# Optimization experiments

Measured on AMD Instinct MI355X. Metric: run time of the kernel, lower is better.

Reference implementation:

```python
import jax, jax.numpy as jnp
import numpy as np

B, T, C, H = 4, 1024, 512, 4
D = C // H
N_LAYER, LAYER_ID = 12, 1


def setup_inputs() -> dict:
    key = jax.random.key(0)
    ks = jax.random.split(key, 10)
    w = lambda k, shape: 0.02 * jax.random.normal(k, shape, dtype=jnp.float32)

    r01 = LAYER_ID / (N_LAYER - 1)          # ratio_0_to_1
    r1a0 = 1.0 - LAYER_ID / N_LAYER          # ratio_1_to_almost0
    i = np.arange(C, dtype=np.float32)
    time_decay = (-5.0 + 8.0 * (i / (C - 1)) ** (0.7 + 1.3 * r01)).astype(np.float32)
    xv = i / C
    tm_q = (xv ** r1a0).astype(np.float32)[None, None, :]
    tm_k = (xv ** r1a0).astype(np.float32)[None, None, :]
    tm_v = ((xv ** r1a0) + 0.3 * r01).astype(np.float32)[None, None, :]
    tm_g = (xv ** (0.5 * r1a0)).astype(np.float32)[None, None, :]

    return dict(
        x=jax.random.normal(ks[0], (B, T, C), dtype=jnp.float32),
        ln1_g=jnp.ones((C,), jnp.float32), ln1_b=jnp.zeros((C,), jnp.float32),
        ln2_g=jnp.ones((C,), jnp.float32), ln2_b=jnp.zeros((C,), jnp.float32),
        time_decay=jnp.asarray(time_decay),
        tm_q=jnp.asarray(tm_q), tm_k=jnp.asarray(tm_k),
        tm_v=jnp.asarray(tm_v), tm_g=jnp.asarray(tm_g),
        Wq=w(ks[1], (C, C)), Wk=w(ks[2], (C, C)), Wv=w(ks[3], (C, C)),
        Wg=w(ks[4], (C, C)), Wo=w(ks[5], (C, C)),
        rms_scale=jnp.ones((C,), jnp.float32),
        W1=w(ks[6], (4 * C, C)), W2=w(ks[7], (C, 4 * C)),
    )


def layernorm(x, g, b, eps=1e-5):
    m = x.mean(-1, keepdims=True)
    v = ((x - m) ** 2).mean(-1, keepdims=True)
    return g * (x - m) / jnp.sqrt(v + eps) + b


def rmsnorm(x, scale, eps=1e-8):
    # matches: norm = ||x||_2 / sqrt(dim); out = scale * x / (norm + eps)
    norm = jnp.sqrt(jnp.sum(x * x, axis=-1, keepdims=True)) / (x.shape[-1] ** 0.5)
    return scale * (x / (norm + eps))


def lnssm_scan(q, k, v, lam):
    """Decayed linear-attention scan. q,k,v: [B,T,H,D]; lam: [H,D] (decay over k index).
    Returns S: [B,T,H,D] = q_t^T A_t, Zs: [B,T,H] = q_t . z_t."""
    qT, kT, vT = (jnp.moveaxis(a, 1, 0) for a in (q, k, v))  # [T,B,H,D]
    Bq = q.shape[0]
    A0 = jnp.zeros((Bq, q.shape[2], q.shape[3], q.shape[3]), q.dtype)
    z0 = jnp.zeros((Bq, q.shape[2], q.shape[3]), q.dtype)

    def step(carry, inp):
        A, z = carry
        qt, kt, vt = inp
        A = lam[None, :, :, None] * A + kt[..., None] * vt[..., None, :]  # [B,H,Dk,Dv]
        z = lam[None] * z + kt                                            # [B,H,Dk]
        St = jnp.einsum('bhi,bhij->bhj', qt, A)
        Zt = jnp.einsum('bhi,bhi->bh', qt, z)
        return (A, z), (St, Zt)

    _, (S, Zs) = jax.lax.scan(step, (A0, z0), (qT, kT, vT))
    return jnp.moveaxis(S, 0, 1), jnp.moveaxis(Zs, 0, 1)


def reference(x, ln1_g, ln1_b, ln2_g, ln2_b, time_decay, tm_q, tm_k, tm_v, tm_g,
              Wq, Wk, Wv, Wg, Wo, rms_scale, W1, W2):
    Bx, Tx, Cx = x.shape
    Hh, Dd = H, Cx // H

    # --- TimeMix on ln1(x) ---
    h = layernorm(x, ln1_g, ln1_b)
    xx = jnp.concatenate([jnp.zeros_like(h[:, :1]), h[:, :-1]], axis=1)  # time shift
    xq = h * tm_q + xx * (1 - tm_q)
    xk = h * tm_k + xx * (1 - tm_k)
    xv_ = h * tm_v + xx * (1 - tm_v)
    xg = h * tm_g + xx * (1 - tm_g)
    q = xq @ Wq.T
    k = xk @ Wk.T
    v = xv_ @ Wv.T
    g = jax.nn.sigmoid(xg @ Wg.T)
    q = jnp.exp(rmsnorm(q, rms_scale))
    k = jnp.exp(rmsnorm(k, rms_scale))

    lam = jnp.exp(-jnp.exp(time_decay)).reshape(Hh, Dd)
    qh = q.reshape(Bx, Tx, Hh, Dd)
    kh = k.reshape(Bx, Tx, Hh, Dd)
    vh = v.reshape(Bx, Tx, Hh, Dd)
    S, Zs = lnssm_scan(qh, kh, vh, lam)
    att = (S / Zs[..., None]).reshape(Bx, Tx, Cx)
    att = (g * att) @ Wo.T
    x = x + att

    # --- ChannelMix on ln2(x) ---
    h2 = layernorm(x, ln2_g, ln2_b)
    x = x + jax.nn.gelu(h2 @ W1.T, approximate=False) @ W2.T
    return x
```

## Files before the change

kernel.cpp:

```cpp
#include <hip/hip_runtime.h>
#include <math.h>

#define Bb 4
#define Tt 1024
#define Cc 512
#define Hh 4
#define Dd 128
#define Mrows (Bb*Tt)
#define NC 32
#define CL 32
#define AUGB_CB 18432

typedef unsigned short u16;
typedef __attribute__((ext_vector_type(8))) short bf16x8;
typedef __attribute__((ext_vector_type(4))) float f32x4;

__device__ __forceinline__ u16 f2bf(float f) {
  unsigned u = __float_as_uint(f);
  unsigned r = (u + 0x7fffu + ((u >> 16) & 1u)) >> 16;
  return (u16)r;
}
__device__ __forceinline__ float bf2f(u16 v) {
  return __uint_as_float((unsigned)v << 16);
}
__device__ __forceinline__ unsigned pack2(float a, float b) {
  return (unsigned)f2bf(a) | ((unsigned)f2bf(b) << 16);
}
__device__ __forceinline__ float rms_r(const float* __restrict__ ssqp, int zsel, int row) {
  const float* p = ssqp + (size_t)zsel*8*Mrows + row;
  float s2 = 0.f;
  #pragma unroll
  for (int u = 0; u < 8; ++u) s2 += p[(size_t)u*Mrows];
  float norm = sqrtf(s2) * 0.044194173824159216f;
  return 1.f / (norm + 1e-8f);
}

__global__ __launch_bounds__(256) void prep_kernel(const float* __restrict__ x,
    const float* __restrict__ g, const float* __restrict__ bta,
    const float* __restrict__ tmq, const float* __restrict__ tmk,
    const float* __restrict__ tmv, const float* __restrict__ tmg,
    u16* __restrict__ xqb, u16* __restrict__ xkb,
    u16* __restrict__ xvb, u16* __restrict__ xgb,
    const float* __restrict__ Wq, const float* __restrict__ Wk,
    const float* __restrict__ Wv, const float* __restrict__ Wg,
    const float* __restrict__ Wo, const float* __restrict__ W1,
    const float* __restrict__ W2, u16* __restrict__ wout)
{
  int tid = threadIdx.x;
  if (blockIdx.x >= 4096) {
    int blk = blockIdx.x - 4096;
    const float* src; u16* dst; int K, nshift;
    if (blk < 640) {
      int wsel = blk >> 7;
      src = wsel==0?Wq:wsel==1?Wk:wsel==2?Wv:wsel==3?Wg:Wo;
      dst = wout + (size_t)wsel*262144; K = 512; nshift = 9; blk &= 127;
    } else if (blk < 1152) {
      src = W1; dst = wout + (size_t)5*262144; K = 512; nshift = 11; blk -= 640;
    } else {
      src = W2; dst = wout + (size_t)5*262144 + 1048576; K = 2048; nshift = 9; blk -= 1152;
    }
    int i = blk*256 + tid;
    int n = i & ((1 << nshift) - 1), kg = i >> nshift;
    const float* p = src + (size_t)n * K + kg * 8;
    float4 a = *(const float4*)p, b = *(const float4*)(p + 4);
    uint4 o;
    o.x = pack2(a.x, a.y); o.y = pack2(a.z, a.w);
    o.z = pack2(b.x, b.y); o.w = pack2(b.z, b.w);
    *(uint4*)(dst + (size_t)i * 8) = o;
    return;
  }
  int m = blockIdx.x;
  const float* xr = x + (size_t)m * Cc;
  float v0 = xr[tid], v1 = xr[tid + 256];
  bool has = (m & (Tt-1)) != 0;
  float u0 = 0.f, u1 = 0.f;
  if (has) { u0 = xr[tid - Cc]; u1 = xr[(int)tid + 256 - Cc]; }
  float sa = v0 + v1, qa = v0*v0 + v1*v1;
  float sb = u0 + u1, qb = u0*u0 + u1*u1;
  #pragma unroll
  for (int off = 32; off > 0; off >>= 1) {
    sa += __shfl_down(sa, off, 64); qa += __shfl_down(qa, off, 64);
    sb += __shfl_down(sb, off, 64); qb += __shfl_down(qb, off, 64);
  }
  __shared__ float r4[4][4];
  int w = tid >> 6;
  if ((tid & 63) == 0) { r4[w][0]=sa; r4[w][1]=qa; r4[w][2]=sb; r4[w][3]=qb; }
  __syncthreads();
  float Sa = r4[0][0]+r4[1][0]+r4[2][0]+r4[3][0];
  float Qa = r4[0][1]+r4[1][1]+r4[2][1]+r4[3][1];
  float Sb = r4[0][2]+r4[1][2]+r4[2][2]+r4[3][2];
  float Qb = r4[0][3]+r4[1][3]+r4[2][3]+r4[3][3];
  float ma = Sa*(1.f/Cc), va = Qa*(1.f/Cc) - ma*ma, ia = rsqrtf(va + 1e-5f);
  float mb = Sb*(1.f/Cc), vb = Qb*(1.f/Cc) - mb*mb, ib = rsqrtf(vb + 1e-5f);
  #pragma unroll
  for (int half = 0; half < 2; ++half) {
    int c = tid + half*256;
    float v = half ? v1 : v0, u = half ? u1 : u0;
    float hv = g[c]*(v - ma)*ia + bta[c];
    float pv = has ? (g[c]*(u - mb)*ib + bta[c]) : 0.f;
    size_t off = ((size_t)(c >> 3) * Mrows + m) * 8 + (c & 7);
    float tq = tmq[c], tk = tmk[c], tv = tmv[c], tg = tmg[c];
    xqb[off] = f2bf(hv*tq + pv*(1.f-tq));
    xkb[off] = f2bf(hv*tk + pv*(1.f-tk));
    xvb[off] = f2bf(hv*tv + pv*(1.f-tv));
    xgb[off] = f2bf(hv*tg + pv*(1.f-tg));
  }
}

__global__ __launch_bounds__(256) void ln2b_kernel(const float* __restrict__ x,
    const float* __restrict__ p0,
    const float* __restrict__ g, const float* __restrict__ bta,
    float* __restrict__ x1, u16* __restrict__ out)
{
  int row = blockIdx.x, tid = threadIdx.x;
  size_t r0 = (size_t)row * Cc + tid, r1 = r0 + 256;
  float v0 = x[r0] + p0[r0];
  float v1 = x[r1] + p0[r1];
  x1[r0] = v0; x1[r1] = v1;
  float s = v0 + v1, s2 = v0*v0 + v1*v1;
  #pragma unroll
  for (int off = 32; off > 0; off >>= 1) {
    s  += __shfl_down(s,  off, 64);
    s2 += __shfl_down(s2, off, 64);
  }
  __shared__ float rs[4], rq[4];
  int w = tid >> 6;
  if ((tid & 63) == 0) { rs[w] = s; rq[w] = s2; }
  __syncthreads();
  float S  = rs[0]+rs[1]+rs[2]+rs[3];
  float S2 = rq[0]+rq[1]+rq[2]+rq[3];
  float mean = S * (1.0f/Cc);
  float var  = S2 * (1.0f/Cc) - mean*mean;
  float inv = rsqrtf(var + 1e-5f);
  int c0 = tid, c1 = tid + 256;
  float o0 = g[c0] * (v0-mean)*inv + bta[c0];
  float o1 = g[c1] * (v1-mean)*inv + bta[c1];
  out[((size_t)(c0 >> 3) * Mrows + row) * 8 + (c0 & 7)] = f2bf(o0);
  out[((size_t)(c1 >> 3) * Mrows + row) * 8 + (c1 & 7)] = f2bf(o1);
}

template<int MR, int NR, int KR>
__device__ __forceinline__ void gemm_core64(const u16* __restrict__ A,
    const u16* __restrict__ W, const float* __restrict__ res,
    float* __restrict__ outf, u16* __restrict__ outb, int act,
    int m0, int n0, u16* Asm, u16* Bsm, float* __restrict__ ssq)
{
  const int tid = threadIdx.x, w = tid >> 6, l = tid & 63;
  const int wr = w >> 1, wc = w & 1;
  f32x4 acc[2][2];
  #pragma unroll
  for (int i = 0; i < 2; ++i)
    #pragma unroll
    for (int j = 0; j < 2; ++j) acc[i][j] = (f32x4){0.f,0.f,0.f,0.f};
  const int kgl = l >> 4, rl = l & 15;
  const int q = w * 2;

  #define STAGE(KT, BUF) do {                                               \
    _Pragma("unroll")                                                       \
    for (int ii = 0; ii < 2; ++ii) {                                        \
      int qq = q + ii;                                                      \
      int isB = qq >> 2, kg = qq & 3;                                       \
      const u16* src = isB                                                  \
        ? W + ((size_t)((KT)*4 + kg) * NR + n0 + l) * 8                     \
        : A + ((size_t)((KT)*4 + kg) * MR + m0 + l) * 8;                    \
      u16* dst = (isB ? Bsm : Asm) + (BUF)*2048 + kg * 64 * 8;              \
      __builtin_amdgcn_global_load_lds(                                     \
          (const __attribute__((address_space(1))) void*)src,               \
          (__attribute__((address_space(3))) void*)dst, 16, 0, 0);          \
    }                                                                       \
  } while (0)

  constexpr int nk = KR >> 5;
  STAGE(0, 0); STAGE(1, 1);
  int cur = 0;
  for (int kt = 0; kt < nk; ++kt) {
    if (kt == nk - 1) asm volatile("s_waitcnt vmcnt(0)" ::: "memory");
    else              asm volatile("s_waitcnt vmcnt(2)" ::: "memory");
    __builtin_amdgcn_s_barrier();
    bf16x8 af[2], bfr[2];
    #pragma unroll
    for (int f = 0; f < 2; ++f)
      af[f] = *(const bf16x8*)&Asm[cur*2048 + (kgl*64 + wr*32 + f*16 + rl) * 8];
    #pragma unroll
    for (int f = 0; f < 2; ++f)
      bfr[f] = *(const bf16x8*)&Bsm[cur*2048 + (kgl*64 + wc*32 + f*16 + rl) * 8];
    if (kt + 2 < nk) {
      int nb = cur + 2; if (nb >= 3) nb -= 3;
      STAGE(kt + 2, nb);
    }
    __builtin_amdgcn_s_setprio(1);
    #pragma unroll
    for (int i = 0; i < 2; ++i)
      #pragma unroll
      for (int j = 0; j < 2; ++j)
        acc[i][j] = __builtin_amdgcn_mfma_f32_16x16x32_bf16(af[i], bfr[j], acc[i][j], 0, 0, 0);
    __builtin_amdgcn_s_setprio(0);
    if (++cur == 3) cur = 0;
  }
  #undef STAGE

  const int rbase = (l >> 4) * 4, cn = l & 15;
  #pragma unroll
  for (int i = 0; i < 2; ++i) {
    #pragma unroll
    for (int j = 0; j < 2; ++j) {
      #pragma unroll
      for (int r = 0; r < 4; ++r) {
        int m = m0 + wr*32 + i*16 + rbase + r;
        int n = n0 + wc*32 + j*16 + cn;
        float vv = acc[i][j][r];
        if (res) vv += res[(size_t)m * NR + n];
        if (act == 1) vv = 0.5f*vv*(1.f + erff(vv * 0.70710678118f));
        else if (act == 2) vv = 1.f/(1.f + expf(-vv));
        if (outb) outb[((size_t)(n >> 3) * MR + m) * 8 + (n & 7)] = f2bf(vv);
        else outf[(size_t)m * NR + n] = vv;
      }
    }
  }

  if (ssq) {
    __syncthreads();
    float* red2 = (float*)Asm;
    #pragma unroll
    for (int i = 0; i < 2; ++i) {
      #pragma unroll
      for (int r = 0; r < 4; ++r) {
        int row_local = wr*32 + i*16 + rbase + r;
        float sq = 0.f;
        #pragma unroll
        for (int j = 0; j < 2; ++j) { float t = acc[i][j][r]; sq += t*t; }
        red2[row_local*32 + wc*16 + cn] = sq;
      }
    }
    __syncthreads();
    if (tid < 64) {
      float ssum = 0.f;
      #pragma unroll
      for (int u2 = 0; u2 < 32; ++u2) ssum += red2[tid*32 + u2];
      ssq[m0 + tid] = ssum;
    }
  }
}

__global__ __launch_bounds__(256) void gemm_qkvg(const u16* __restrict__ xall,
    const u16* __restrict__ Wall, float* __restrict__ outall, float* __restrict__ ssqp)
{
  __shared__ __align__(16) u16 Asm[3*2048];
  __shared__ __align__(16) u16 Bsm[3*2048];
  int z = blockIdx.z;
  const size_t E = (size_t)Mrows * Cc;
  float* ssq = (z < 2) ? ssqp + ((size_t)z*8 + blockIdx.x)*Mrows : nullptr;
  gemm_core64<Mrows,512,512>(xall + z*E, Wall + (size_t)z*262144, nullptr,
            outall + z*E, nullptr, z == 3 ? 2 : 0,
            blockIdx.y * 64, blockIdx.x * 64, Asm, Bsm, ssq);
}

__global__ __launch_bounds__(256) void gemm_wo(const u16* __restrict__ A,
    const u16* __restrict__ W, float* __restrict__ outf)
{
  __shared__ __align__(16) u16 Asm[3*2048];
  __shared__ __align__(16) u16 Bsm[3*2048];
  gemm_core64<Mrows,512,512>(A, W, nullptr, outf, nullptr, 0,
            blockIdx.y * 64, blockIdx.x * 64, Asm, Bsm, nullptr);
}

__global__ __launch_bounds__(256) void gemm_w1(const u16* __restrict__ A,
    const u16* __restrict__ W, u16* __restrict__ outb)
{
  __shared__ __align__(16) u16 Asm[3*2048];
  __shared__ __align__(16) u16 Bsm[3*2048];
  gemm_core64<Mrows,2048,512>(A, W, nullptr, nullptr, outb, 1,
            blockIdx.y * 64, blockIdx.x * 64, Asm, Bsm, nullptr);
}

__global__ __launch_bounds__(256) void gemm_w2(const u16* __restrict__ A,
    const u16* __restrict__ W, float* __restrict__ pbuf)
{
  __shared__ __align__(16) u16 Asm[3*2048];
  __shared__ __align__(16) u16 Bsm[3*2048];
  int z = blockIdx.z;
  const size_t E = (size_t)Mrows * Cc;
  gemm_core64<Mrows,512,1024>(A + (size_t)z*128*Mrows*8, W + (size_t)z*128*512*8, nullptr,
            pbuf + z*E, nullptr, 0, blockIdx.y * 64, blockIdx.x * 64, Asm, Bsm, nullptr);
}

__global__ __launch_bounds__(256) void reduce2_kernel(const float* __restrict__ x1,
    const float* __restrict__ p, float* __restrict__ out)
{
  const size_t E = (size_t)Mrows * Cc;
  size_t f = ((size_t)blockIdx.x * 256 + threadIdx.x) * 4;
  float4 a = *(const float4*)(x1 + f);
  float4 q0 = *(const float4*)(p + f);
  float4 q1 = *(const float4*)(p + E + f);
  float4 o;
  o.x = a.x + q0.x + q1.x;
  o.y = a.y + q0.y + q1.y;
  o.z = a.z + q0.z + q1.z;
  o.w = a.w + q0.w + q1.w;
  *(float4*)(out + f) = o;
}

__global__ __launch_bounds__(256) void chunk_state_kernel(const float* __restrict__ k,
    const float* __restrict__ v, const float* __restrict__ td,
    const float* __restrict__ rsc, const float* __restrict__ ssqp,
    u16* __restrict__ Augl)
{
  __shared__ float k_lds[CL][Dd];
  __shared__ float v_lds[CL][Dd];
  int blk = blockIdx.x; int c = blk & (NC-1); int bh = blk >> 5;
  int b = bh >> 2, h = bh & 3;
  int tid = threadIdx.x;
  size_t base = ((size_t)b*Tt + (size_t)c*CL)*Cc + h*Dd;
  #pragma unroll
  for (int r = 0; r < 4; ++r) {
    int idx4 = r*256 + tid;
    int s = idx4 >> 5; int i4 = (idx4 & 31) << 2;
    float rk = rms_r(ssqp, 1, b*Tt + c*CL + s);
    float4 kr = *(const float4*)&k[base + (size_t)s*Cc + i4];
    k_lds[s][i4+0] = expf(rsc[h*Dd+i4+0] * kr.x * rk);
    k_lds[s][i4+1] = expf(rsc[h*Dd+i4+1] * kr.y * rk);
    k_lds[s][i4+2] = expf(rsc[h*Dd+i4+2] * kr.z * rk);
    k_lds[s][i4+3] = expf(rsc[h*Dd+i4+3] * kr.w * rk);
    *(float4*)&v_lds[s][i4] = *(const float4*)&v[base + (size_t)s*Cc + i4];
  }
  __syncthreads();
  int iq = tid >> 3; int i0 = iq << 2;
  int jg = tid & 7;  int j0 = jg << 4;
  float lam4[4], powv[4], zacc[4];
  #pragma unroll
  for (int ci=0; ci<4; ++ci) {
    lam4[ci] = expf(-expf(td[h*Dd + i0 + ci]));
    powv[ci] = 1.f; zacc[ci] = 0.f;
  }
  float acc[4][16];
  #pragma unroll
  for (int ci=0; ci<4; ++ci)
    #pragma unroll
    for (int jj=0; jj<16; ++jj) acc[ci][jj] = 0.f;

  for (int s = CL-1; s >= 0; --s) {
    float4 k4 = *(const float4*)&k_lds[s][i0];
    float kw0 = powv[0]*k4.x, kw1 = powv[1]*k4.y, kw2 = powv[2]*k4.z, kw3 = powv[3]*k4.w;
    zacc[0]+=kw0; zacc[1]+=kw1; zacc[2]+=kw2; zacc[3]+=kw3;
    #pragma unroll
    for (int q4 = 0; q4 < 4; ++q4) {
      float4 v4 = *(const float4*)&v_lds[s][j0 + q4*4];
      float vv[4] = {v4.x, v4.y, v4.z, v4.w};
      #pragma unroll
      for (int u=0; u<4; ++u) {
        acc[0][q4*4+u] += kw0*vv[u];
        acc[1][q4*4+u] += kw1*vv[u];
        acc[2][q4*4+u] += kw2*vv[u];
        acc[3][q4*4+u] += kw3*vv[u];
      }
    }
    powv[0]*=lam4[0]; powv[1]*=lam4[1]; powv[2]*=lam4[2]; powv[3]*=lam4[3];
  }
  u16* aug = Augl + ((size_t)c*16 + bh)*AUGB_CB;
  const int ig = i0 >> 3, isub = i0 & 7;
  #pragma unroll
  for (int jj=0; jj<16; ++jj) {
    int j = j0 + jj;
    uint2 pk;
    pk.x = pack2(acc[0][jj], acc[1][jj]);
    pk.y = pack2(acc[2][jj], acc[3][jj]);
    *(uint2*)&aug[(size_t)ig*1152 + (size_t)j*8 + isub] = pk;
  }
  if (jg == 0) {
    uint2 pk;
    pk.x = pack2(zacc[0], zacc[1]);
    pk.y = pack2(zacc[2], zacc[3]);
    *(uint2*)&aug[(size_t)ig*1152 + 128*8 + isub] = pk;
  }
}

__global__ __launch_bounds__(256) void combine_kernel(const u16* __restrict__ Augl,
    const float* __restrict__ td, u16* __restrict__ Augb)
{
  int idx = blockIdx.x*256 + threadIdx.x;
  if (idx >= 129*128) return;
  int bh = blockIdx.y; int h = bh & 3;
  int j = idx >> 7, i = idx & 127;
  size_t aoff = (size_t)(i >> 3) * 1152 + (size_t)j * 8 + (i & 7);
  float lamL = expf(-expf(td[h*Dd + i]) * (float)CL);
  const u16* pl = Augl + (size_t)bh*AUGB_CB + aoff;
  u16* pi = Augb + (size_t)bh*AUGB_CB + aoff;
  float prev = 0.f;
  const size_t cstr = (size_t)16*AUGB_CB;
  for (int c = 0; c < NC; ++c) {
    float val = bf2f(pl[c*cstr]);
    pi[c*cstr] = f2bf(prev);
    prev = lamL*prev + val;
  }
}

__global__ __launch_bounds__(256, 2) void scan_mfma_kernel(
    const float* __restrict__ q, const float* __restrict__ k,
    const float* __restrict__ v, const float* __restrict__ td,
    const float* __restrict__ rsc, const float* __restrict__ ssqp,
    const u16* __restrict__ Augb, const float* __restrict__ gmat,
    u16* __restrict__ out)
{
  __shared__ float k_lds[32*192];
  __shared__ u16  qfrag[32*128];
  __shared__ u16  vfrag[4*1152];
  __shared__ float P32[32*33];
  __shared__ u16  pfrag[32*32];
  __shared__ float lam_lds[128];
  __shared__ float zbuf[32];

  const int tid = threadIdx.x;
  const int blk = blockIdx.x; const int c = blk & 31, bh = blk >> 5;
  const int b = bh >> 2, h = bh & 3;
  const int w = tid >> 6, l = tid & 63;
  const int t = (w << 3) + (l >> 3);
  const int is = l & 7;

  if (tid < 128) lam_lds[tid] = expf(-expf(td[h*Dd + tid]));

  const int grow = b*Tt + c*CL + t;
  const size_t rowbase = ((size_t)grow)*Cc + h*Dd + is*16;
  const float rq = rms_r(ssqp, 0, grow);
  const float rk = rms_r(ssqp, 1, grow);

  float qv[16];
  {
    #pragma unroll
    for (int c4 = 0; c4 < 4; ++c4) {
      float4 q4 = *(const float4*)(q + rowbase + c4*4);
      int e0 = c4*4;
      qv[e0+0] = expf(rsc[h*Dd+is*16+e0+0] * q4.x * rq);
      qv[e0+1] = expf(rsc[h*Dd+is*16+e0+1] * q4.y * rq);
      qv[e0+2] = expf(rsc[h*Dd+is*16+e0+2] * q4.z * rq);
      qv[e0+3] = expf(rsc[h*Dd+is*16+e0+3] * q4.w * rq);
    }
    float lt = (float)(t + 1);
    u16 qt[16];
    #pragma unroll
    for (int e = 0; e < 16; ++e) {
      float el2 = -expf(td[h*Dd + is*16 + e]) * 1.4426950408889634f;
      qt[e] = f2bf(qv[e] * exp2f(el2 * lt));
    }
    #pragma unroll
    for (int hf = 0; hf < 2; ++hf) {
      int k8 = is*2 + hf;
      uint4 pk;
      pk.x = (unsigned)qt[hf*8+0] | ((unsigned)qt[hf*8+1]<<16);
      pk.y = (unsigned)qt[hf*8+2] | ((unsigned)qt[hf*8+3]<<16);
      pk.z = (unsigned)qt[hf*8+4] | ((unsigned)qt[hf*8+5]<<16);
      pk.w = (unsigned)qt[hf*8+6] | ((unsigned)qt[hf*8+7]<<16);
      *(uint4*)&qfrag[t*128 + ((k8 ^ (t&7))<<3)] = pk;
    }
  }
  #pragma unroll
  for (int c4 = 0; c4 < 4; ++c4) {
    float4 k4 = *(const float4*)(k + rowbase + c4*4);
    int e0 = is*16 + c4*4;
    k_lds[t*192 + is*24 + c4*4+0] = expf(rsc[h*Dd+e0+0] * k4.x * rk);
    k_lds[t*192 + is*24 + c4*4+1] = expf(rsc[h*Dd+e0+1] * k4.y * rk);
    k_lds[t*192 + is*24 + c4*4+2] = expf(rsc[h*Dd+e0+2] * k4.z * rk);
    k_lds[t*192 + is*24 + c4*4+3] = expf(rsc[h*Dd+e0+3] * k4.w * rk);
  }
  #pragma unroll
  for (int c4 = 0; c4 < 4; ++c4) {
    float4 v4 = *(const float4*)(v + rowbase + c4*4);
    int j0 = is*16 + c4*4;
    vfrag[(t>>3)*1152 + (j0+0)*8 + (t&7)] = f2bf(v4.x);
    vfrag[(t>>3)*1152 + (j0+1)*8 + (t&7)] = f2bf(v4.y);
    vfrag[(t>>3)*1152 + (j0+2)*8 + (t&7)] = f2bf(v4.z);
    vfrag[(t>>3)*1152 + (j0+3)*8 + (t&7)] = f2bf(v4.w);
  }
  if (tid < 32) vfrag[(tid>>3)*1152 + 128*8 + (tid&7)] = 0x3F80;
  if (tid < 240) {
    #pragma unroll
    for (int u = 0; u < 2; ++u) {
      int e = tid*2 + u;
      int ig = e / 120, rem = e % 120;
      vfrag[ig*1152 + (129 + rem/8)*8 + (rem&7)] = 0;
    }
  }
  __syncthreads();

  {
    float lamr[16], wrun[16];
    #pragma unroll
    for (int e4 = 0; e4 < 4; ++e4) {
      float4 l4 = *(const float4*)&lam_lds[is*16 + e4*4];
      lamr[e4*4+0]=l4.x; lamr[e4*4+1]=l4.y; lamr[e4*4+2]=l4.z; lamr[e4*4+3]=l4.w;
    }
    #pragma unroll
    for (int e = 0; e < 16; ++e) wrun[e] = 1.f;
    const int smax = (w << 3) + 7;
    for (int s = smax; s >= 0; --s) {
      float dot = 0.f;
      #pragma unroll
      for (int c4 = 0; c4 < 4; ++c4) {
        float4 k4 = *(const float4*)&k_lds[s*192 + is*24 + c4*4];
        dot = fmaf(qv[c4*4+0], k4.x*wrun[c4*4+0], dot);
        dot = fmaf(qv[c4*4+1], k4.y*wrun[c4*4+1], dot);
        dot = fmaf(qv[c4*4+2], k4.z*wrun[c4*4+2], dot);
        dot = fmaf(qv[c4*4+3], k4.w*wrun[c4*4+3], dot);
      }
      dot += __shfl_xor(dot, 1);
      dot += __shfl_xor(dot, 2);
      dot += __shfl_xor(dot, 4);
      bool act = (s <= t);
      if (act && is == 0) P32[t*33 + s] = dot;
      if (act) {
        #pragma unroll
        for (int e = 0; e < 16; ++e) wrun[e] *= lamr[e];
      }
    }
  }
  __syncthreads();
  {
    int tt = tid >> 3, s0 = (tid & 7) * 4;
    #pragma unroll
    for (int ss = 0; ss < 4; ++ss) {
      int s = s0 + ss;
      float val = (s <= tt) ? P32[tt*33 + s] : 0.f;
      pfrag[tt*32 + (((s>>3) ^ (tt&3))<<3) + (s&7)] = f2bf(val);
    }
  }
  __syncthreads();

  const int tau = w >> 1;
  const int jt0 = (w & 1) ? 5 : 0;
  const int njt = (w & 1) ? 4 : 5;
  const int rl = l & 15, kg = l >> 4;
  const int trow = tau*16 + rl;
  const u16* augb_base = Augb + ((size_t)c*16 + bh)*AUGB_CB;

  bf16x8 aq[4];
  #pragma unroll
  for (int kk = 0; kk < 4; ++kk)
    aq[kk] = *(const bf16x8*)&qfrag[trow*128 + ((((kk<<2)+kg) ^ (trow&7))<<3)];
  bf16x8 ap = *(const bf16x8*)&pfrag[trow*32 + ((kg ^ (trow&3))<<3)];

  f32x4 acc[5];
  #pragma unroll
  for (int u = 0; u < 5; ++u) acc[u] = (f32x4){0.f,0.f,0.f,0.f};

  #pragma unroll
  for (int u = 0; u < 5; ++u) {
    if (u < njt) {
      int jt = jt0 + u;
      #pragma unroll
      for (int kk = 0; kk < 4; ++kk) {
        bf16x8 bfr = *(const bf16x8*)&augb_base[(size_t)(((kk<<2)+kg)*1152 + (jt*16 + rl)*8)];
        acc[u] = __builtin_amdgcn_mfma_f32_16x16x32_bf16(aq[kk], bfr, acc[u], 0, 0, 0);
      }
      bf16x8 bv = *(const bf16x8*)&vfrag[kg*1152 + (jt*16 + rl)*8];
      acc[u] = __builtin_amdgcn_mfma_f32_16x16x32_bf16(ap, bv, acc[u], 0, 0, 0);
    }
  }
  if ((w & 1) && rl == 0) {
    #pragma unroll
    for (int r = 0; r < 4; ++r) zbuf[tau*16 + kg*4 + r] = acc[3][r];
  }
  __syncthreads();

  const int nout = (w & 1) ? 3 : 5;
  #pragma unroll
  for (int u = 0; u < 5; ++u) {
    if (u < nout) {
      int jt = jt0 + u;
      int cc = h*Dd + jt*16 + rl;
      #pragma unroll
      for (int r = 0; r < 4; ++r) {
        int tr = tau*16 + kg*4 + r;
        int m = b*Tt + c*CL + tr;
        float zv = zbuf[tr];
        float gv = gmat[(size_t)m*Cc + cc];
        out[((size_t)(cc >> 3) * Mrows + m) * 8 + (cc & 7)] = f2bf(gv * acc[u][r] / zv);
      }
    }
  }
}

extern "C" void kernel_launch(void* const* d_in, const int* in_sizes, int n_in,
                              void* d_out, int out_size, void* d_ws, size_t ws_size,
                              hipStream_t stream) {
  const float* x    = (const float*)d_in[0];
  const float* ln1g = (const float*)d_in[1];
  const float* ln1b = (const float*)d_in[2];
  const float* ln2g = (const float*)d_in[3];
  const float* ln2b = (const float*)d_in[4];
  const float* td   = (const float*)d_in[5];
  const float* tmq  = (const float*)d_in[6];
  const float* tmk  = (const float*)d_in[7];
  const float* tmv  = (const float*)d_in[8];
  const float* tmg  = (const float*)d_in[9];
  const float* Wq   = (const float*)d_in[10];
  const float* Wk   = (const float*)d_in[11];
  const float* Wv   = (const float*)d_in[12];
  const float* Wg   = (const float*)d_in[13];
  const float* Wo   = (const float*)d_in[14];
  const float* rsc  = (const float*)d_in[15];
  const float* W1   = (const float*)d_in[16];
  const float* W2   = (const float*)d_in[17];
  float* ws = (float*)d_ws;
  const size_t E = (size_t)Mrows*Cc;
  float* s0 = ws;
  float* s1 = ws + E;
  float* s2 = ws + 2*E;
  float* s3 = ws + 3*E;
  float* x1 = ws + 4*E;
  u16* xqb = (u16*)(ws + 5*E);
  u16* xkb = xqb + E;
  u16* xvb = xkb + E;
  u16* xgb = xvb + E;
  u16* wreg = (u16*)(ws + 7*E);
  u16* Wqb = wreg;
  u16* Wob = wreg + 4*262144;
  u16* W1b = wreg + 5*262144;
  u16* W2b = W1b + 1048576;
  u16* Augl = W2b + 1048576;
  u16* Augb = Augl + (size_t)NC*16*AUGB_CB;
  float* ssqp = (float*)(Augb + (size_t)NC*16*AUGB_CB);
  u16* midb  = Augl;
  u16* gattb = xqb;
  u16* h2b   = xkb;

  prep_kernel<<<5760,256,0,stream>>>(x, ln1g, ln1b, tmq,tmk,tmv,tmg,
                                     xqb,xkb,xvb,xgb,
                                     Wq, Wk, Wv, Wg, Wo, W1, W2, Wqb);
  gemm_qkvg<<<dim3(8,64,4),256,0,stream>>>(xqb, Wqb, s0, ssqp);
  chunk_state_kernel<<<16*NC,256,0,stream>>>(s1, s2, td, rsc, ssqp, Augl);
  combine_kernel<<<dim3(65,16),256,0,stream>>>(Augl, td, Augb);
  scan_mfma_kernel<<<16*NC,256,0,stream>>>(s0, s1, s2, td, rsc, ssqp, Augb, s3, gattb);
  gemm_wo<<<dim3(8,64),256,0,stream>>>(gattb, Wob, s2);
  ln2b_kernel<<<Mrows,256,0,stream>>>(x, s2, ln2g, ln2b, x1, h2b);
  gemm_w1<<<dim3(32,64),256,0,stream>>>(h2b, W1b, midb);
  gemm_w2<<<dim3(8,64,2),256,0,stream>>>(midb, W2b, s0);
  reduce2_kernel<<<2048,256,0,stream>>>(x1, s0, (float*)d_out);
}
```

Baseline: 173.3 us.

## Emit bf16 blocked q/k/v/g from projection GEMM and fuse residual into W2 GEMM

The QKVG projection GEMM now writes bf16 output in the blocked k-group layout instead of fp32 row-major. chunk_state and scan kernels read and unpack these bf16 values, which halves the traffic for q, k, v and g. The W2 GEMM no longer splits K into two partial buffers followed by a reduce kernel. It runs the full K=2048 with the residual fused into its epilogue, removing one launch and the partial-sum traffic. The costs are extra bf16 rounding of q/k/v/g before the exp and the scan, and half as many blocks in the W2 GEMM.

```diff
diff --git a/kernel.cpp b/kernel.cpp
--- a/kernel.cpp
+++ b/kernel.cpp
@@ -25,6 +25,12 @@
 }
 __device__ __forceinline__ unsigned pack2(float a, float b) {
   return (unsigned)f2bf(a) | ((unsigned)f2bf(b) << 16);
+}
+__device__ __forceinline__ void unpack8(uint4 a, u16* o) {
+  o[0]=(u16)a.x; o[1]=(u16)(a.x>>16);
+  o[2]=(u16)a.y; o[3]=(u16)(a.y>>16);
+  o[4]=(u16)a.z; o[5]=(u16)(a.z>>16);
+  o[6]=(u16)a.w; o[7]=(u16)(a.w>>16);
 }
 __device__ __forceinline__ float rms_r(const float* __restrict__ ssqp, int zsel, int row) {
   const float* p = ssqp + (size_t)zsel*8*Mrows + row;
@@ -76,22 +82,22 @@
   float u0 = 0.f, u1 = 0.f;
   if (has) { u0 = xr[tid - Cc]; u1 = xr[(int)tid + 256 - Cc]; }
   float sa = v0 + v1, qa = v0*v0 + v1*v1;
-  float sb = u0 + u1, qb = u0*u0 + u1*u1;
+  float sb = u0 + u1, qb2 = u0*u0 + u1*u1;
   #pragma unroll
   for (int off = 32; off > 0; off >>= 1) {
     sa += __shfl_down(sa, off, 64); qa += __shfl_down(qa, off, 64);
-    sb += __shfl_down(sb, off, 64); qb += __shfl_down(qb, off, 64);
+    sb += __shfl_down(sb, off, 64); qb2 += __shfl_down(qb2, off, 64);
   }
   __shared__ float r4[4][4];
   int w = tid >> 6;
-  if ((tid & 63) == 0) { r4[w][0]=sa; r4[w][1]=qa; r4[w][2]=sb; r4[w][3]=qb; }
+  if ((tid & 63) == 0) { r4[w][0]=sa; r4[w][1]=qa; r4[w][2]=sb; r4[w][3]=qb2; }
   __syncthreads();
   float Sa = r4[0][0]+r4[1][0]+r4[2][0]+r4[3][0];
   float Qa = r4[0][1]+r4[1][1]+r4[2][1]+r4[3][1];
   float Sb = r4[0][2]+r4[1][2]+r4[2][2]+r4[3][2];
   float Qb = r4[0][3]+r4[1][3]+r4[2][3]+r4[3][3];
   float ma = Sa*(1.f/Cc), va = Qa*(1.f/Cc) - ma*ma, ia = rsqrtf(va + 1e-5f);
-  float mb = Sb*(1.f/Cc), vb = Qb*(1.f/Cc) - mb*mb, ib = rsqrtf(vb + 1e-5f);
+  float mb = Sb*(1.f/Cc), vb2 = Qb*(1.f/Cc) - mb*mb, ib = rsqrtf(vb2 + 1e-5f);
   #pragma unroll
   for (int half = 0; half < 2; ++half) {
     int c = tid + half*256;
@@ -243,7 +249,7 @@
 }
 
 __global__ __launch_bounds__(256) void gemm_qkvg(const u16* __restrict__ xall,
-    const u16* __restrict__ Wall, float* __restrict__ outall, float* __restrict__ ssqp)
+    const u16* __restrict__ Wall, u16* __restrict__ outall, float* __restrict__ ssqp)
 {
   __shared__ __align__(16) u16 Asm[3*2048];
   __shared__ __align__(16) u16 Bsm[3*2048];
@@ -251,7 +257,7 @@
   const size_t E = (size_t)Mrows * Cc;
   float* ssq = (z < 2) ? ssqp + ((size_t)z*8 + blockIdx.x)*Mrows : nullptr;
   gemm_core64<Mrows,512,512>(xall + z*E, Wall + (size_t)z*262144, nullptr,
-            outall + z*E, nullptr, z == 3 ? 2 : 0,
+            nullptr, outall + z*E, z == 3 ? 2 : 0,
             blockIdx.y * 64, blockIdx.x * 64, Asm, Bsm, ssq);
 }
 
@@ -274,34 +280,16 @@
 }
 
 __global__ __launch_bounds__(256) void gemm_w2(const u16* __restrict__ A,
-    const u16* __restrict__ W, float* __restrict__ pbuf)
+    const u16* __restrict__ W, const float* __restrict__ res, float* __restrict__ outf)
 {
   __shared__ __align__(16) u16 Asm[3*2048];
   __shared__ __align__(16) u16 Bsm[3*2048];
-  int z = blockIdx.z;
-  const size_t E = (size_t)Mrows * Cc;
-  gemm_core64<Mrows,512,1024>(A + (size_t)z*128*Mrows*8, W + (size_t)z*128*512*8, nullptr,
-            pbuf + z*E, nullptr, 0, blockIdx.y * 64, blockIdx.x * 64, Asm, Bsm, nullptr);
-}
-
-__global__ __launch_bounds__(256) void reduce2_kernel(const float* __restrict__ x1,
-    const float* __restrict__ p, float* __restrict__ out)
-{
-  const size_t E = (size_t)Mrows * Cc;
-  size_t f = ((size_t)blockIdx.x * 256 + threadIdx.x) * 4;
-  float4 a = *(const float4*)(x1 + f);
-  float4 q0 = *(const float4*)(p + f);
-  float4 q1 = *(const float4*)(p + E + f);
-  float4 o;
-  o.x = a.x + q0.x + q1.x;
-  o.y = a.y + q0.y + q1.y;
-  o.z = a.z + q0.z + q1.z;
-  o.w = a.w + q0.w + q1.w;
-  *(float4*)(out + f) = o;
-}
-
-__global__ __launch_bounds__(256) void chunk_state_kernel(const float* __restrict__ k,
-    const float* __restrict__ v, const float* __restrict__ td,
+  gemm_core64<Mrows,512,2048>(A, W, res, outf, nullptr, 0,
+            blockIdx.y * 64, blockIdx.x * 64, Asm, Bsm, nullptr);
+}
+
+__global__ __launch_bounds__(256) void chunk_state_kernel(const u16* __restrict__ kb,
+    const u16* __restrict__ vb, const float* __restrict__ td,
     const float* __restrict__ rsc, const float* __restrict__ ssqp,
     u16* __restrict__ Augl)
 {
@@ -310,18 +298,24 @@
   int blk = blockIdx.x; int c = blk & (NC-1); int bh = blk >> 5;
   int b = bh >> 2, h = bh & 3;
   int tid = threadIdx.x;
-  size_t base = ((size_t)b*Tt + (size_t)c*CL)*Cc + h*Dd;
   #pragma unroll
   for (int r = 0; r < 4; ++r) {
     int idx4 = r*256 + tid;
     int s = idx4 >> 5; int i4 = (idx4 & 31) << 2;
-    float rk = rms_r(ssqp, 1, b*Tt + c*CL + s);
-    float4 kr = *(const float4*)&k[base + (size_t)s*Cc + i4];
-    k_lds[s][i4+0] = expf(rsc[h*Dd+i4+0] * kr.x * rk);
-    k_lds[s][i4+1] = expf(rsc[h*Dd+i4+1] * kr.y * rk);
-    k_lds[s][i4+2] = expf(rsc[h*Dd+i4+2] * kr.z * rk);
-    k_lds[s][i4+3] = expf(rsc[h*Dd+i4+3] * kr.w * rk);
-    *(float4*)&v_lds[s][i4] = *(const float4*)&v[base + (size_t)s*Cc + i4];
+    int m = b*Tt + c*CL + s;
+    float rk = rms_r(ssqp, 1, m);
+    int cidx = h*Dd + i4;
+    size_t boff = ((size_t)(cidx >> 3) * Mrows + m) * 8 + (cidx & 7);
+    uint2 kr = *(const uint2*)(kb + boff);
+    uint2 vr = *(const uint2*)(vb + boff);
+    k_lds[s][i4+0] = expf(rsc[h*Dd+i4+0] * bf2f((u16)kr.x) * rk);
+    k_lds[s][i4+1] = expf(rsc[h*Dd+i4+1] * bf2f((u16)(kr.x>>16)) * rk);
+    k_lds[s][i4+2] = expf(rsc[h*Dd+i4+2] * bf2f((u16)kr.y) * rk);
+    k_lds[s][i4+3] = expf(rsc[h*Dd+i4+3] * bf2f((u16)(kr.y>>16)) * rk);
+    v_lds[s][i4+0] = bf2f((u16)vr.x);
+    v_lds[s][i4+1] = bf2f((u16)(vr.x>>16));
+    v_lds[s][i4+2] = bf2f((u16)vr.y);
+    v_lds[s][i4+3] = bf2f((u16)(vr.y>>16));
   }
   __syncthreads();
   int iq = tid >> 3; int i0 = iq << 2;
@@ -395,10 +389,10 @@
 }
 
 __global__ __launch_bounds__(256, 2) void scan_mfma_kernel(
-    const float* __restrict__ q, const float* __restrict__ k,
-    const float* __restrict__ v, const float* __restrict__ td,
+    const u16* __restrict__ qb, const u16* __restrict__ kb,
+    const u16* __restrict__ vb, const float* __restrict__ td,
     const float* __restrict__ rsc, const float* __restrict__ ssqp,
-    const u16* __restrict__ Augb, const float* __restrict__ gmat,
+    const u16* __restrict__ Augb, const u16* __restrict__ gb,
     u16* __restrict__ out)
 {
   __shared__ float k_lds[32*192];
@@ -419,21 +413,20 @@
   if (tid < 128) lam_lds[tid] = expf(-expf(td[h*Dd + tid]));
 
   const int grow = b*Tt + c*CL + t;
-  const size_t rowbase = ((size_t)grow)*Cc + h*Dd + is*16;
   const float rq = rms_r(ssqp, 0, grow);
   const float rk = rms_r(ssqp, 1, grow);
+  const int g0 = (h*Dd + is*16) >> 3;
+  const size_t bbase = ((size_t)g0*Mrows + grow)*8;
 
   float qv[16];
   {
-    #pragma unroll
-    for (int c4 = 0; c4 < 4; ++c4) {
-      float4 q4 = *(const float4*)(q + rowbase + c4*4);
-      int e0 = c4*4;
-      qv[e0+0] = expf(rsc[h*Dd+is*16+e0+0] * q4.x * rq);
-      qv[e0+1] = expf(rsc[h*Dd+is*16+e0+1] * q4.y * rq);
-      qv[e0+2] = expf(rsc[h*Dd+is*16+e0+2] * q4.z * rq);
-      qv[e0+3] = expf(rsc[h*Dd+is*16+e0+3] * q4.w * rq);
-    }
+    uint4 qA = *(const uint4*)(qb + bbase);
+    uint4 qB = *(const uint4*)(qb + bbase + (size_t)Mrows*8);
+    u16 qraw[16];
+    unpack8(qA, qraw); unpack8(qB, qraw + 8);
+    #pragma unroll
+    for (int e = 0; e < 16; ++e)
+      qv[e] = expf(rsc[h*Dd + is*16 + e] * bf2f(qraw[e]) * rq);
     float lt = (float)(t + 1);
     u16 qt[16];
     #pragma unroll
@@ -452,23 +445,23 @@
       *(uint4*)&qfrag[t*128 + ((k8 ^ (t&7))<<3)] = pk;
     }
   }
-  #pragma unroll
-  for (int c4 = 0; c4 < 4; ++c4) {
-    float4 k4 = *(const float4*)(k + rowbase + c4*4);
-    int e0 = is*16 + c4*4;
-    k_lds[t*192 + is*24 + c4*4+0] = expf(rsc[h*Dd+e0+0] * k4.x * rk);
-    k_lds[t*192 + is*24 + c4*4+1] = expf(rsc[h*Dd+e0+1] * k4.y * rk);
-    k_lds[t*192 + is*24 + c4*4+2] = expf(rsc[h*Dd+e0+2] * k4.z * rk);
-    k_lds[t*192 + is*24 + c4*4+3] = expf(rsc[h*Dd+e0+3] * k4.w * rk);
-  }
-  #pragma unroll
-  for (int c4 = 0; c4 < 4; ++c4) {
-    float4 v4 = *(const float4*)(v + rowbase + c4*4);
-    int j0 = is*16 + c4*4;
-    vfrag[(t>>3)*1152 + (j0+0)*8 + (t&7)] = f2bf(v4.x);
-    vfrag[(t>>3)*1152 + (j0+1)*8 + (t&7)] = f2bf(v4.y);
-    vfrag[(t>>3)*1152 + (j0+2)*8 + (t&7)] = f2bf(v4.z);
-    vfrag[(t>>3)*1152 + (j0+3)*8 + (t&7)] = f2bf(v4.w);
+  {
+    uint4 kA = *(const uint4*)(kb + bbase);
+    uint4 kB = *(const uint4*)(kb + bbase + (size_t)Mrows*8);
+    u16 kraw[16];
+    unpack8(kA, kraw); unpack8(kB, kraw + 8);
+    #pragma unroll
+    for (int e = 0; e < 16; ++e)
+      k_lds[t*192 + is*24 + e] = expf(rsc[h*Dd + is*16 + e] * bf2f(kraw[e]) * rk);
+  }
+  {
+    uint4 vA = *(const uint4*)(vb + bbase);
+    uint4 vB = *(const uint4*)(vb + bbase + (size_t)Mrows*8);
+    u16 vraw[16];
+    unpack8(vA, vraw); unpack8(vB, vraw + 8);
+    #pragma unroll
+    for (int e = 0; e < 16; ++e)
+      vfrag[(t>>3)*1152 + (is*16 + e)*8 + (t&7)] = vraw[e];
   }
   if (tid < 32) vfrag[(tid>>3)*1152 + 128*8 + (tid&7)] = 0x3F80;
   if (tid < 240) {
@@ -571,7 +564,7 @@
         int tr = tau*16 + kg*4 + r;
         int m = b*Tt + c*CL + tr;
         float zv = zbuf[tr];
-        float gv = gmat[(size_t)m*Cc + cc];
+        float gv = bf2f(gb[((size_t)(cc >> 3) * Mrows + m) * 8 + (cc & 7)]);
         out[((size_t)(cc >> 3) * Mrows + m) * 8 + (cc & 7)] = f2bf(gv * acc[u][r] / zv);
       }
     }
@@ -601,19 +594,20 @@
   const float* W2   = (const float*)d_in[17];
   float* ws = (float*)d_ws;
   const size_t E = (size_t)Mrows*Cc;
-  float* s0 = ws;
-  float* s1 = ws + E;
-  float* s2 = ws + 2*E;
-  float* s3 = ws + 3*E;
-  float* x1 = ws + 4*E;
-  u16* xqb = (u16*)(ws + 5*E);
+  float* x1 = ws;
+  float* s2 = ws + E;
+  u16* ub  = (u16*)(ws + 2*E);
+  u16* xqb = ub;
   u16* xkb = xqb + E;
   u16* xvb = xkb + E;
   u16* xgb = xvb + E;
-  u16* wreg = (u16*)(ws + 7*E);
-  u16* Wqb = wreg;
-  u16* Wob = wreg + 4*262144;
-  u16* W1b = wreg + 5*262144;
+  u16* qb  = ub + 4*E;
+  u16* kb  = qb + E;
+  u16* vb  = kb + E;
+  u16* gb  = vb + E;
+  u16* Wqb = ub + 8*E;
+  u16* Wob = Wqb + 4*262144;
+  u16* W1b = Wqb + 5*262144;
   u16* W2b = W1b + 1048576;
   u16* Augl = W2b + 1048576;
   u16* Augb = Augl + (size_t)NC*16*AUGB_CB;
@@ -625,13 +619,12 @@
   prep_kernel<<<5760,256,0,stream>>>(x, ln1g, ln1b, tmq,tmk,tmv,tmg,
                                      xqb,xkb,xvb,xgb,
                                      Wq, Wk, Wv, Wg, Wo, W1, W2, Wqb);
-  gemm_qkvg<<<dim3(8,64,4),256,0,stream>>>(xqb, Wqb, s0, ssqp);
-  chunk_state_kernel<<<16*NC,256,0,stream>>>(s1, s2, td, rsc, ssqp, Augl);
+  gemm_qkvg<<<dim3(8,64,4),256,0,stream>>>(xqb, Wqb, qb, ssqp);
+  chunk_state_kernel<<<16*NC,256,0,stream>>>(kb, vb, td, rsc, ssqp, Augl);
   combine_kernel<<<dim3(65,16),256,0,stream>>>(Augl, td, Augb);
-  scan_mfma_kernel<<<16*NC,256,0,stream>>>(s0, s1, s2, td, rsc, ssqp, Augb, s3, gattb);
+  scan_mfma_kernel<<<16*NC,256,0,stream>>>(qb, kb, vb, td, rsc, ssqp, Augb, gb, gattb);
   gemm_wo<<<dim3(8,64),256,0,stream>>>(gattb, Wob, s2);
   ln2b_kernel<<<Mrows,256,0,stream>>>(x, s2, ln2g, ln2b, x1, h2b);
   gemm_w1<<<dim3(32,64),256,0,stream>>>(h2b, W1b, midb);
-  gemm_w2<<<dim3(8,64,2),256,0,stream>>>(midb, W2b, s0);
-  reduce2_kernel<<<2048,256,0,stream>>>(x1, s0, (float*)d_out);
-}
+  gemm_w2<<<dim3(8,64),256,0,stream>>>(midb, W2b, x1, (float*)d_out);
+}
```

New measurement: 169.5 us. 1.02x faster.
